# Kernel tuning notes

Hardware: AMD Instinct MI355X
Metric: run time of the kernel (lower is better)

## Reference

```python
import jax, jax.numpy as jnp
import numpy as np

NUM_CLASSES = 2
IGNORE_INDEX = 2


def setup_inputs() -> dict:
    key = jax.random.key(0)
    k1, k2 = jax.random.split(key)
    probs = jax.random.uniform(k1, (2, 2, 32, 512, 512), dtype=jnp.float32)  # (B,C,D,H,W)
    gt_mask = jax.random.randint(k2, (2, 32, 512, 512), 0, 3, dtype=jnp.int32)  # (B,D,H,W), includes ignore_index=2
    return {"probs": probs, "gt_mask": gt_mask}


def _one_hot_target(gt_mask):
    # ignore_index -> 0, clamp to [0, NUM_CLASSES-1], one-hot to channel axis 1
    gt = jnp.where(gt_mask == IGNORE_INDEX, 0, gt_mask)
    gt = jnp.clip(gt, 0, NUM_CLASSES - 1)
    oh = jax.nn.one_hot(gt, NUM_CLASSES, dtype=jnp.float32)  # (B,D,H,W,C)
    return jnp.moveaxis(oh, -1, 1)  # (B,C,D,H,W)


def reference(probs, gt_mask):
    # Per-z-slice 2D loss (surrogate for the opaque topological _loss_2d:
    # mean squared error between probs and one-hot target per slice),
    # vectorized over the z loop, then 'mean' reduction over slices.
    oh = _one_hot_target(gt_mask)  # (B,C,D,H,W)
    per_z = jnp.mean((probs - oh) ** 2, axis=(0, 1, 3, 4))  # (D,)
    return jnp.mean(per_z)
```

## Files before the change

kernel.cpp:

```cpp
#include <hip/hip_runtime.h>
#include <stdint.h>

static constexpr long long DHW       = 32LL * 512 * 512;
static constexpr long long N_SPATIAL = 2LL * DHW;
static constexpr long long N_TOTAL   = 2LL * N_SPATIAL;

static constexpr int GRID   = 1024;
static constexpr int BLOCK  = 256;
static constexpr int ROUNDS = 16;
static constexpr long long CHUNKS  = N_SPATIAL / 4;
static constexpr long long RSTRIDE = (long long)GRID * BLOCK;
static_assert(CHUNKS == (long long)ROUNDS * RSTRIDE, "exact trip count");

typedef float fx4 __attribute__((ext_vector_type(4)));
typedef int   ix4 __attribute__((ext_vector_type(4)));

__device__ __forceinline__ void stage16(const void* g, void* lds) {
    __builtin_amdgcn_global_load_lds(
        (const __attribute__((address_space(1))) void*)g,
        (__attribute__((address_space(3))) void*)lds,
        16, 0, 0);
}

__global__ __launch_bounds__(BLOCK) void betti_mse_partial(const float* __restrict__ probs,
                                                           const int*   __restrict__ mask,
                                                           double*      __restrict__ partial) {
    __shared__ float lp0[2][BLOCK * 4];
    __shared__ float lp1[2][BLOCK * 4];
    __shared__ int   lm [2][BLOCK * 4];

    const int tid  = threadIdx.x;
    const int wseg = (tid >> 6) << 8;

    float a0 = 0.0f, a1 = 0.0f;

    auto stage = [&](int buf, int r) {
        const long long v    = (long long)r * RSTRIDE + (long long)blockIdx.x * BLOCK + tid;
        const long long s    = v << 2;
        const long long b    = s >> 23;
        const long long base = (b << 24) + (s & (DHW - 1));
        stage16(probs + base,       &lp0[buf][wseg]);
        stage16(probs + base + DHW, &lp1[buf][wseg]);
        stage16(mask + s,           &lm [buf][wseg]);
    };

    auto consume = [&](int buf) {
        const fx4 p0 = *reinterpret_cast<const fx4*>(&lp0[buf][tid << 2]);
        const fx4 p1 = *reinterpret_cast<const fx4*>(&lp1[buf][tid << 2]);
        const ix4 m  = *reinterpret_cast<const ix4*>(&lm [buf][tid << 2]);
        const float t0 = (m.x == 1) ? 1.0f : 0.0f;
        const float t1 = (m.y == 1) ? 1.0f : 0.0f;
        const float t2 = (m.z == 1) ? 1.0f : 0.0f;
        const float t3 = (m.w == 1) ? 1.0f : 0.0f;
        float d;
        d = p0.x - (1.0f - t0); a0 += d * d;
        d = p0.y - (1.0f - t1); a1 += d * d;
        d = p0.z - (1.0f - t2); a0 += d * d;
        d = p0.w - (1.0f - t3); a1 += d * d;
        d = p1.x - t0;          a0 += d * d;
        d = p1.y - t1;          a1 += d * d;
        d = p1.z - t2;          a0 += d * d;
        d = p1.w - t3;          a1 += d * d;
    };

    stage(0, 0);
    for (int r = 0; r < ROUNDS - 1; ++r) {
        stage((r + 1) & 1, r + 1);
        __builtin_amdgcn_s_waitcnt(0x0F73);
        __asm__ __volatile__("" ::: "memory");
        consume(r & 1);
        __asm__ __volatile__("" ::: "memory");
    }
    __builtin_amdgcn_s_waitcnt(0x0F70);
    __asm__ __volatile__("" ::: "memory");
    consume((ROUNDS - 1) & 1);

    float local = a0 + a1;
    #pragma unroll
    for (int off = 32; off > 0; off >>= 1)
        local += __shfl_down(local, off, 64);

    __shared__ float wsum[4];
    const int lane = tid & 63;
    const int wid  = tid >> 6;
    if (lane == 0) wsum[wid] = local;
    __syncthreads();
    if (tid == 0)
        partial[blockIdx.x] = (double)(wsum[0] + wsum[1] + wsum[2] + wsum[3]);
}

__global__ __launch_bounds__(BLOCK) void betti_mse_final(const double* __restrict__ partial,
                                                         float* __restrict__ out) {
    double local = 0.0;
    #pragma unroll
    for (int k = 0; k < GRID / BLOCK; ++k)
        local += partial[threadIdx.x + k * BLOCK];

    #pragma unroll
    for (int off = 32; off > 0; off >>= 1)
        local += __shfl_down(local, off, 64);

    __shared__ double wsum[4];
    const int lane = threadIdx.x & 63;
    const int wid  = threadIdx.x >> 6;
    if (lane == 0) wsum[wid] = local;
    __syncthreads();
    if (threadIdx.x == 0)
        out[0] = (float)((wsum[0] + wsum[1] + wsum[2] + wsum[3]) / (double)N_TOTAL);
}

extern "C" void kernel_launch(void* const* d_in, const int* in_sizes, int n_in,
                              void* d_out, int out_size, void* d_ws, size_t ws_size,
                              hipStream_t stream) {
    const float* probs   = (const float*)d_in[0];
    const int*   mask    = (const int*)d_in[1];
    float*       out     = (float*)d_out;
    double*      partial = (double*)d_ws;

    betti_mse_partial<<<GRID, BLOCK, 0, stream>>>(probs, mask, partial);
    betti_mse_final<<<1, BLOCK, 0, stream>>>(partial, out);
}
```

Before: 231.3 us.

## Load probs directly into registers with nontemporal loads, stage only mask via LDS

```diff
diff --git a/kernel.cpp b/kernel.cpp
--- a/kernel.cpp
+++ b/kernel.cpp
@@ -1,13 +1,12 @@
 #include <hip/hip_runtime.h>
-#include <stdint.h>
 
 static constexpr long long DHW       = 32LL * 512 * 512;
 static constexpr long long N_SPATIAL = 2LL * DHW;
 static constexpr long long N_TOTAL   = 2LL * N_SPATIAL;
 
-static constexpr int GRID   = 1024;
+static constexpr int GRID   = 2048;
 static constexpr int BLOCK  = 256;
-static constexpr int ROUNDS = 16;
+static constexpr int ROUNDS = 8;
 static constexpr long long CHUNKS  = N_SPATIAL / 4;
 static constexpr long long RSTRIDE = (long long)GRID * BLOCK;
 static_assert(CHUNKS == (long long)ROUNDS * RSTRIDE, "exact trip count");
@@ -25,55 +24,60 @@
 __global__ __launch_bounds__(BLOCK) void betti_mse_partial(const float* __restrict__ probs,
                                                            const int*   __restrict__ mask,
                                                            double*      __restrict__ partial) {
-    __shared__ float lp0[2][BLOCK * 4];
-    __shared__ float lp1[2][BLOCK * 4];
-    __shared__ int   lm [2][BLOCK * 4];
+    __shared__ int lm[2][BLOCK * 4];
 
     const int tid  = threadIdx.x;
     const int wseg = (tid >> 6) << 8;
 
-    float a0 = 0.0f, a1 = 0.0f;
-
-    auto stage = [&](int buf, int r) {
-        const long long v    = (long long)r * RSTRIDE + (long long)blockIdx.x * BLOCK + tid;
-        const long long s    = v << 2;
-        const long long b    = s >> 23;
-        const long long base = (b << 24) + (s & (DHW - 1));
-        stage16(probs + base,       &lp0[buf][wseg]);
-        stage16(probs + base + DHW, &lp1[buf][wseg]);
-        stage16(mask + s,           &lm [buf][wseg]);
+    auto sidx = [&](int r) -> long long {
+        return ((long long)r * RSTRIDE + (long long)blockIdx.x * BLOCK + tid) << 2;
+    };
+    auto probs_base = [&](long long s) -> long long {
+        return ((s >> 23) << 24) + (s & (DHW - 1));
     };
 
-    auto consume = [&](int buf) {
-        const fx4 p0 = *reinterpret_cast<const fx4*>(&lp0[buf][tid << 2]);
-        const fx4 p1 = *reinterpret_cast<const fx4*>(&lp1[buf][tid << 2]);
-        const ix4 m  = *reinterpret_cast<const ix4*>(&lm [buf][tid << 2]);
+    float a0 = 0.0f, a1 = 0.0f;
+    fx4 p0c, p1c, p0n, p1n;
+
+    {
+        const long long s = sidx(0);
+        stage16(mask + s, &lm[0][wseg]);
+        const long long base = probs_base(s);
+        p0c = __builtin_nontemporal_load(reinterpret_cast<const fx4*>(probs + base));
+        p1c = __builtin_nontemporal_load(reinterpret_cast<const fx4*>(probs + base + DHW));
+    }
+
+    for (int r = 0; r < ROUNDS; ++r) {
+        if (r + 1 < ROUNDS) {
+            const long long s = sidx(r + 1);
+            stage16(mask + s, &lm[(r + 1) & 1][wseg]);
+            const long long base = probs_base(s);
+            p0n = __builtin_nontemporal_load(reinterpret_cast<const fx4*>(probs + base));
+            p1n = __builtin_nontemporal_load(reinterpret_cast<const fx4*>(probs + base + DHW));
+        }
+        __asm__ __volatile__("" ::: "memory");
+        if (r + 1 < ROUNDS) __builtin_amdgcn_s_waitcnt(0x0F73);
+        else                __builtin_amdgcn_s_waitcnt(0x0F70);
+        __asm__ __volatile__("" ::: "memory");
+
+        const ix4 m = *reinterpret_cast<const ix4*>(&lm[r & 1][tid << 2]);
         const float t0 = (m.x == 1) ? 1.0f : 0.0f;
         const float t1 = (m.y == 1) ? 1.0f : 0.0f;
         const float t2 = (m.z == 1) ? 1.0f : 0.0f;
         const float t3 = (m.w == 1) ? 1.0f : 0.0f;
         float d;
-        d = p0.x - (1.0f - t0); a0 += d * d;
-        d = p0.y - (1.0f - t1); a1 += d * d;
-        d = p0.z - (1.0f - t2); a0 += d * d;
-        d = p0.w - (1.0f - t3); a1 += d * d;
-        d = p1.x - t0;          a0 += d * d;
-        d = p1.y - t1;          a1 += d * d;
-        d = p1.z - t2;          a0 += d * d;
-        d = p1.w - t3;          a1 += d * d;
-    };
+        d = p0c.x - (1.0f - t0); a0 += d * d;
+        d = p0c.y - (1.0f - t1); a1 += d * d;
+        d = p0c.z - (1.0f - t2); a0 += d * d;
+        d = p0c.w - (1.0f - t3); a1 += d * d;
+        d = p1c.x - t0;          a0 += d * d;
+        d = p1c.y - t1;          a1 += d * d;
+        d = p1c.z - t2;          a0 += d * d;
+        d = p1c.w - t3;          a1 += d * d;
 
-    stage(0, 0);
-    for (int r = 0; r < ROUNDS - 1; ++r) {
-        stage((r + 1) & 1, r + 1);
-        __builtin_amdgcn_s_waitcnt(0x0F73);
-        __asm__ __volatile__("" ::: "memory");
-        consume(r & 1);
-        __asm__ __volatile__("" ::: "memory");
+        p0c = p0n;
+        p1c = p1n;
     }
-    __builtin_amdgcn_s_waitcnt(0x0F70);
-    __asm__ __volatile__("" ::: "memory");
-    consume((ROUNDS - 1) & 1);
 
     float local = a0 + a1;
     #pragma unroll
```

After: 221.9 us. 4.1% less time.
